# Performance work log

Hardware: AMD Instinct MI355X
Metric: run time of the kernel (lower is better)

## Reference

```python
import jax, jax.numpy as jnp
import numpy as np
import math

F = 64        # num_features (multiplicity of each irrep)
N = 16000     # nodes
E = 256000    # edges (avg_num_neighbors = 16)
S = 4         # num_species
DE = 32       # scalar edge feature dim (radial basis)
W = 128       # interaction_mlp_width
AVG_NEIGH = 16.0
SQ2 = math.sqrt(2.0)
SQ3 = math.sqrt(3.0)


def setup_inputs() -> dict:
    key = jax.random.key(0)
    ks = jax.random.split(key, 32)
    def nrm(k, shape, scale=1.0):
        return jax.random.normal(k, shape, dtype=jnp.float32) * scale
    inp = {}
    # forward args
    inp["vectors"] = nrm(ks[0], (E, 1, 3))
    inp["lengths"] = jax.random.uniform(ks[1], (E, 1), dtype=jnp.float32)
    inp["node_s"] = nrm(ks[2], (N, F))            # 64x0e part of node_feats
    inp["node_v"] = nrm(ks[3], (N, F, 3))         # 64x1o part of node_feats
    inp["scalar_edge_feats"] = nrm(ks[4], (E, DE))
    inp["node_specie"] = jax.random.randint(ks[5], (N,), 0, S)
    inp["senders"] = jax.random.randint(ks[6], (E,), 0, N)
    inp["receivers"] = jax.random.randint(ks[7], (E,), 0, N)
    # parameters (e3nn Linear = per-irrep channel mixing, fan-in normalized; bias only on 0e)
    inp["W_up_s"] = nrm(ks[8], (F, F), F ** -0.5); inp["b_up_s"] = jnp.zeros((F,), jnp.float32)
    inp["W_up_v"] = nrm(ks[9], (F, F), F ** -0.5)
    din = 2 * F + DE + 1
    inp["mlp_W1"] = nrm(ks[10], (din, W), din ** -0.5); inp["mlp_b1"] = jnp.zeros((W,), jnp.float32)
    inp["mlp_W2"] = nrm(ks[11], (W, W), W ** -0.5); inp["mlp_b2"] = jnp.zeros((W,), jnp.float32)
    inp["mlp_W3"] = nrm(ks[12], (W, 3 * F), W ** -0.5); inp["mlp_b3"] = jnp.zeros((3 * F,), jnp.float32)
    inp["W_dn_s"] = nrm(ks[13], (F, F), F ** -0.5); inp["b_dn_s"] = jnp.zeros((F,), jnp.float32)
    inp["W_dn_v"] = nrm(ks[14], (2 * F, F), (2 * F) ** -0.5)
    # symmetric contraction weights (per species, per channel); correlation=2
    inp["w_sc_s"] = nrm(ks[15], (S, 3, F), 3 ** -0.5)   # paths to 0e: x0, x0^2, (x1.x1)/sqrt3
    inp["w_sc_v"] = nrm(ks[16], (S, 2, F), 2 ** -0.5)   # paths to 1o: x1, x0*x1
    inp["W_pb_s"] = nrm(ks[17], (F, F), F ** -0.5); inp["b_pb_s"] = jnp.zeros((F,), jnp.float32)
    inp["W_pb_v"] = nrm(ks[18], (F, F), F ** -0.5)
    inp["W_r1_s"] = nrm(ks[19], (F, 2 * F), F ** -0.5); inp["b_r1_s"] = jnp.zeros((2 * F,), jnp.float32)
    inp["W_r1_v"] = nrm(ks[20], (F, F), F ** -0.5)
    inp["W_r2_s"] = nrm(ks[21], (F, 1), F ** -0.5); inp["b_r2"] = jnp.zeros((1,), jnp.float32)
    inp["W_r2_v"] = nrm(ks[22], (F, 1), F ** -0.5)
    return inp


def reference(vectors, lengths, node_s, node_v, scalar_edge_feats, node_specie,
              senders, receivers,
              W_up_s, b_up_s, W_up_v,
              mlp_W1, mlp_b1, mlp_W2, mlp_b2, mlp_W3, mlp_b3,
              W_dn_s, b_dn_s, W_dn_v,
              w_sc_s, w_sc_v, W_pb_s, b_pb_s, W_pb_v,
              W_r1_s, b_r1_s, W_r1_v, W_r2_s, b_r2, W_r2_v):
    n = node_s.shape[0]
    # --- spherical harmonics, sh_irreps='1o', component normalization, normalize=False ---
    edge_v = SQ3 * vectors[:, 0, :]                              # [E,3]

    # --- InteractionBlock: linear_up ---
    h_s = node_s @ W_up_s + b_up_s                               # [N,F]
    h_v = jnp.einsum('nfi,fg->ngi', node_v, W_up_v)              # [N,F,3]

    # --- MessagePassingConvolution ---
    m_s = h_s[senders]                                           # [E,F] 0e
    m_v = h_v[senders]                                           # [E,F,3] 1o
    # tensor product with edge 1o, filtered to 0e+1o (unitary CG):
    tp_s = jnp.einsum('efi,ei->ef', m_v, edge_v) / SQ3           # 1o x 1o -> 0e  [E,F]
    tp_v1 = m_s[:, :, None] * edge_v[:, None, :]                 # 0e x 1o -> 1o  [E,F,3]
    tp_v2 = jnp.cross(m_v, edge_v[:, None, :]) / SQ2             # 1o x 1o -> 1o  [E,F,3]
    # scalar MLP mix (one scalar weight per output irrep = 3F)
    mlp_in = jnp.concatenate([m_s, h_s[receivers], scalar_edge_feats, lengths], axis=1)
    h = jax.nn.silu(mlp_in @ mlp_W1 + mlp_b1)
    h = jax.nn.silu(h @ mlp_W2 + mlp_b2)
    mix = h @ mlp_W3 + mlp_b3                                    # [E,3F]
    mix_s, mix_v1, mix_v2 = mix[:, :F], mix[:, F:2 * F], mix[:, 2 * F:]
    tp_s = tp_s * mix_s
    tp_v = jnp.concatenate([tp_v1 * mix_v1[:, :, None], tp_v2 * mix_v2[:, :, None]], axis=1)  # [E,2F,3]
    # scatter-add to receivers, normalize by avg_num_neighbors
    agg_s = jax.ops.segment_sum(tp_s, receivers, num_segments=n) / AVG_NEIGH   # [N,F]
    agg_v = jax.ops.segment_sum(tp_v, receivers, num_segments=n) / AVG_NEIGH   # [N,2F,3]
    # linear_down
    f_s = agg_s @ W_dn_s + b_dn_s                                # [N,F]
    f_v = jnp.einsum('nfi,fg->ngi', agg_v, W_dn_v)               # [N,F,3]

    # --- EquivariantProductBasisBlock: symmetric contraction (correlation=2), per-species ---
    ws = w_sc_s[node_specie]                                     # [N,3,F]
    wv = w_sc_v[node_specie]                                     # [N,2,F]
    vv = jnp.sum(f_v * f_v, axis=-1) / SQ3                       # 1o (x) 1o -> 0e, symmetric
    sc_s = ws[:, 0] * f_s + ws[:, 1] * (f_s * f_s) + ws[:, 2] * vv           # [N,F]
    sc_v = wv[:, 0][:, :, None] * f_v + wv[:, 1][:, :, None] * (f_s[:, :, None] * f_v)  # [N,F,3]
    p_s = sc_s @ W_pb_s + b_pb_s                                 # node_feats 0e out
    p_v = jnp.einsum('nfi,fg->ngi', sc_v, W_pb_v)                # node_feats 1o out

    # --- NonLinearReadoutBlock: linear to (2F x 0e + F x 1o), gate, linear to 1x0e+1x1o ---
    r_s = p_s @ W_r1_s + b_r1_s                                  # [N,2F]
    r_v = jnp.einsum('nfi,fg->ngi', p_v, W_r1_v)                 # [N,F,3]
    act = jax.nn.silu(r_s[:, :F])
    gates = jax.nn.silu(r_s[:, F:])
    g_v = gates[:, :, None] * r_v                                # gated vectors
    out_s = act @ W_r2_s + b_r2                                  # [N,1]  0e output
    out_v = jnp.einsum('nfi,fo->noi', g_v, W_r2_v)               # [N,1,3] 1o output
    return out_s, out_v, p_s, p_v
```

## Files before the change

### kernel.cpp

```cpp
#include <hip/hip_runtime.h>

typedef short bf16x8 __attribute__((ext_vector_type(8)));
typedef float f32x4  __attribute__((ext_vector_type(4)));
typedef unsigned short ushort_t;

__device__ __forceinline__ float silu(float x) {
    float t = __expf(-x);
    return x * __builtin_amdgcn_rcpf(1.f + t);
}

__device__ __forceinline__ ushort_t f2bs(float x) {
    union { float f; unsigned int u; } v; v.f = x;
    unsigned int r = v.u + 0x7FFF + ((v.u >> 16) & 1);
    return (ushort_t)(r >> 16);
}
__device__ __forceinline__ ushort_t f2bs_t(float x) {
    union { float f; unsigned int u; } v; v.f = x;
    return (ushort_t)(v.u >> 16);
}
__device__ __forceinline__ float bs2f(ushort_t x) {
    union { unsigned int u; float f; } v; v.u = ((unsigned int)x) << 16; return v.f;
}

#define BAR_LGKM() do { \
    asm volatile("s_waitcnt lgkmcnt(0)" ::: "memory"); \
    __builtin_amdgcn_s_barrier(); \
} while (0)

constexpr int N_   = 16000;
constexpr int E_   = 256000;
constexpr int Fd   = 64;

constexpr float SQ3f    = 1.7320508075688772f;
constexpr float INV_SQ3 = 0.5773502691896258f;
constexpr float INV_SQ2 = 0.7071067811865476f;
constexpr float INV_AVG = 0.0625f;

constexpr int OFF_OS = 0;
constexpr int OFF_OV = N_;
constexpr int OFF_PS = OFF_OV + 3 * N_;
constexpr int OFF_PV = OFF_PS + N_ * Fd;

constexpr int W1P_SZ = 6 * 8 * 512;
constexpr int W2P_SZ = 4 * 8 * 512;
constexpr int W3P_SZ = 4 * 12 * 512;

constexpr int AGG_W = 448;

constexpr int H2_OFF = 8704;

__global__ __launch_bounds__(256) void pack_kernel(
    const float* __restrict__ W1, const float* __restrict__ W2,
    const float* __restrict__ W3,
    ushort_t* __restrict__ W1p, ushort_t* __restrict__ W2p,
    ushort_t* __restrict__ W3p)
{
    int idx = blockIdx.x * 256 + threadIdx.x;
    if (idx < W1P_SZ) {
        int j = idx & 7, lane = (idx >> 3) & 63, tile = idx >> 9;
        int c = tile >> 3, t = tile & 7;
        int k = c * 32 + (lane >> 4) * 8 + j;
        int n = t * 16 + (lane & 15);
        W1p[idx] = f2bs(k < 161 ? W1[k * 128 + n] : 0.f);
    } else if (idx < W1P_SZ + W2P_SZ) {
        int q = idx - W1P_SZ;
        int j = q & 7, lane = (q >> 3) & 63, tile = q >> 9;
        int c = tile >> 3, t = tile & 7;
        int k = c * 32 + (lane >> 4) * 8 + j;
        int n = t * 16 + (lane & 15);
        W2p[q] = f2bs(W2[k * 128 + n]);
    } else {
        int q = idx - W1P_SZ - W2P_SZ;
        int j = q & 7, lane = (q >> 3) & 63, tile = q >> 9;
        int c = tile / 12, t = tile % 12;
        int k = c * 32 + (lane >> 4) * 8 + j;
        int n = t * 16 + (lane & 15);
        W3p[q] = f2bs(W3[k * 192 + n]);
    }
}

__global__ __launch_bounds__(64, 4) void up_kernel(
    const float* __restrict__ node_s, const float* __restrict__ node_v,
    const float* __restrict__ W_up_s, const float* __restrict__ b_up_s,
    const float* __restrict__ W_up_v,
    const int* __restrict__ receivers, int* __restrict__ cnt,
    ushort_t* __restrict__ hs_bf, float* __restrict__ h_v)
{
    __shared__ float ns[4][64];
    __shared__ float nv[4][64][3];
    const int n0 = blockIdx.x * 4;
    const int g  = threadIdx.x;

    {
        int e = blockIdx.x * 64 + g;
        atomicAdd(&cnt[receivers[e]], 1);
    }

    #pragma unroll
    for (int j = 0; j < 4; j++) ns[j][g] = node_s[(n0 + j) * 64 + g];
    for (int idx = g; idx < 4 * 192; idx += 64) {
        int j = idx / 192, r = idx - j * 192;
        nv[j][r / 3][r % 3] = node_v[(size_t)n0 * 192 + idx];
    }
    __syncthreads();

    float as[4], a0[4], a1[4], a2[4];
    float bb = b_up_s[g];
    #pragma unroll
    for (int j = 0; j < 4; j++) { as[j] = bb; a0[j] = a1[j] = a2[j] = 0.f; }
    #pragma unroll 4
    for (int f = 0; f < 64; f++) {
        float wss = W_up_s[f * 64 + g];
        float wv  = W_up_v[f * 64 + g];
        #pragma unroll
        for (int j = 0; j < 4; j++) {
            as[j] += ns[j][f] * wss;
            a0[j] += nv[j][f][0] * wv;
            a1[j] += nv[j][f][1] * wv;
            a2[j] += nv[j][f][2] * wv;
        }
    }
    #pragma unroll
    for (int j = 0; j < 4; j++) {
        hs_bf[(n0 + j) * 64 + g] = f2bs(as[j]);
        h_v[(n0 + j) * 192 + 0 * 64 + g] = a0[j];
        h_v[(n0 + j) * 192 + 1 * 64 + g] = a1[j];
        h_v[(n0 + j) * 192 + 2 * 64 + g] = a2[j];
    }
}

__global__ __launch_bounds__(1024) void scan_kernel(
    const int* __restrict__ cnt, int* __restrict__ base, int* __restrict__ cursor)
{
    __shared__ int part[1024];
    const int t = threadIdx.x;
    int v[16];
    int s = 0;
    if (t < 1000) {
        const int4* c4 = (const int4*)(cnt + t * 16);
        #pragma unroll
        for (int q = 0; q < 4; q++) {
            int4 w = c4[q];
            v[q * 4 + 0] = w.x; v[q * 4 + 1] = w.y;
            v[q * 4 + 2] = w.z; v[q * 4 + 3] = w.w;
            s += w.x + w.y + w.z + w.w;
        }
    }
    part[t] = s;
    __syncthreads();
    for (int off = 1; off < 1024; off <<= 1) {
        int u = (t >= off) ? part[t - off] : 0;
        __syncthreads();
        part[t] += u;
        __syncthreads();
    }
    if (t < 1000) {
        int run = part[t] - s;
        int b[16];
        #pragma unroll
        for (int i = 0; i < 16; i++) { b[i] = run; run += v[i]; }
        int4* bb = (int4*)(base + t * 16);
        int4* cc = (int4*)(cursor + t * 16);
        #pragma unroll
        for (int q = 0; q < 4; q++) {
            int4 w = { b[q * 4], b[q * 4 + 1], b[q * 4 + 2], b[q * 4 + 3] };
            bb[q] = w;
            cc[q] = w;
        }
    }
}

__global__ __launch_bounds__(256) void perm_kernel(
    const int* __restrict__ receivers, int* __restrict__ cursor,
    int* __restrict__ eid)
{
    int e = blockIdx.x * 256 + threadIdx.x;
    int r = receivers[e];
    int p = atomicAdd(&cursor[r], 1);
    eid[p] = e;
}

__global__ __launch_bounds__(256, 4) void edge_mlp_kernel(
    const float* __restrict__ lengths, const float* __restrict__ sef,
    const int* __restrict__ senders, const int* __restrict__ receivers,
    const float* __restrict__ vectors, const int* __restrict__ eid,
    const float* __restrict__ b1f, const float* __restrict__ b2f,
    const float* __restrict__ b3f,
    const ushort_t* __restrict__ hs_bf, const float* __restrict__ h_v,
    const ushort_t* __restrict__ W1p, const ushort_t* __restrict__ W2p,
    const ushort_t* __restrict__ W3p,
    float* __restrict__ agg)
{
    __shared__ ushort_t U[17408];
    __shared__ int snd_s[64];
    __shared__ int rcv_s[64];
    __shared__ float ev_s[64][3];

    const int tid  = threadIdx.x;
    const int wave = tid >> 6, lane = tid & 63;
    const int quad = lane >> 4, l4 = lane & 15;
    const int e0   = blockIdx.x * 64;

    if (tid < 64) {
        int e = eid[e0 + tid];
        snd_s[tid] = senders[e];
        rcv_s[tid] = receivers[e];
        ev_s[tid][0] = SQ3f * vectors[e * 3 + 0];
        ev_s[tid][1] = SQ3f * vectors[e * 3 + 1];
        ev_s[tid][2] = SQ3f * vectors[e * 3 + 2];
    }

    {
        const int e  = tid & 63;
        const int ge = eid[e0 + e];
        const int snd = senders[ge];
        const int rcv = receivers[ge];
        for (int c = tid >> 6; c < 24; c += 4) {
            bf16x8 v;
            if (c < 8) {
                v = *(const bf16x8*)(hs_bf + snd * 64 + c * 8);
            } else if (c < 16) {
                v = *(const bf16x8*)(hs_bf + rcv * 64 + (c - 8) * 8);
            } else if (c < 20) {
                const float4 s0 = *(const float4*)(sef + (size_t)ge * 32 + (c - 16) * 8);
                const float4 s1 = *(const float4*)(sef + (size_t)ge * 32 + (c - 16) * 8 + 4);
                v[0] = (short)f2bs(s0.x); v[1] = (short)f2bs(s0.y);
                v[2] = (short)f2bs(s0.z); v[3] = (short)f2bs(s0.w);
                v[4] = (short)f2bs(s1.x); v[5] = (short)f2bs(s1.y);
                v[6] = (short)f2bs(s1.z); v[7] = (short)f2bs(s1.w);
            } else if (c == 20) {
                v = (bf16x8){0,0,0,0,0,0,0,0};
                v[0] = (short)f2bs(lengths[ge]);
            } else {
                v = (bf16x8){0,0,0,0,0,0,0,0};
            }
            *(bf16x8*)(&U[e * 200 + c * 8]) = v;
        }
    }
    BAR_LGKM();

    const bf16x8* B1 = (const bf16x8*)W1p;
    const bf16x8* B2 = (const bf16x8*)W2p;
    const bf16x8* B3 = (const bf16x8*)W3p;

    {
        f32x4 acc[2][4];
        #pragma unroll
        for (int ti = 0; ti < 2; ti++)
            #pragma unroll
            for (int m = 0; m < 4; m++) acc[ti][m] = (f32x4){0,0,0,0};
        #pragma unroll
        for (int c = 0; c < 6; c++) {
            bf16x8 b0 = B1[(c * 8 + wave * 2 + 0) * 64 + lane];
            bf16x8 b1 = B1[(c * 8 + wave * 2 + 1) * 64 + lane];
            #pragma unroll
            for (int m = 0; m < 4; m++) {
                bf16x8 a = *(const bf16x8*)(&U[(m * 16 + l4) * 200 + c * 32 + quad * 8]);
                acc[0][m] = __builtin_amdgcn_mfma_f32_16x16x32_bf16(a, b0, acc[0][m], 0, 0, 0);
                acc[1][m] = __builtin_amdgcn_mfma_f32_16x16x32_bf16(a, b1, acc[1][m], 0, 0, 0);
            }
        }
        BAR_LGKM();
        #pragma unroll
        for (int ti = 0; ti < 2; ti++) {
            int t = wave * 2 + ti;
            float bb = b1f[t * 16 + l4];
            #pragma unroll
            for (int m = 0; m < 4; m++)
                #pragma unroll
                for (int r = 0; r < 4; r++)
                    U[(m * 16 + quad * 4 + r) * 136 + t * 16 + l4] =
                        f2bs_t(silu(acc[ti][m][r] + bb));
        }
    }
    BAR_LGKM();

    {
        f32x4 acc[2][4];
        #pragma unroll
        for (int ti = 0; ti < 2; ti++)
            #pragma unroll
            for (int m = 0; m < 4; m++) acc[ti][m] = (f32x4){0,0,0,0};
        #pragma unroll
        for (int c = 0; c < 4; c++) {
            bf16x8 b0 = B2[(c * 8 + wave * 2 + 0) * 64 + lane];
            bf16x8 b1 = B2[(c * 8 + wave * 2 + 1) * 64 + lane];
            #pragma unroll
            for (int m = 0; m < 4; m++) {
                bf16x8 a = *(const bf16x8*)(&U[(m * 16 + l4) * 136 + c * 32 + quad * 8]);
                acc[0][m] = __builtin_amdgcn_mfma_f32_16x16x32_bf16(a, b0, acc[0][m], 0, 0, 0);
                acc[1][m] = __builtin_amdgcn_mfma_f32_16x16x32_bf16(a, b1, acc[1][m], 0, 0, 0);
            }
        }
        #pragma unroll
        for (int ti = 0; ti < 2; ti++) {
            int t = wave * 2 + ti;
            float bb = b2f[t * 16 + l4];
            #pragma unroll
            for (int m = 0; m < 4; m++)
                #pragma unroll
                for (int r = 0; r < 4; r++)
                    U[H2_OFF + (m * 16 + quad * 4 + r) * 136 + t * 16 + l4] =
                        f2bs_t(silu(acc[ti][m][r] + bb));
        }
    }
    BAR_LGKM();

    {
        f32x4 acc[3][4];
        #pragma unroll
        for (int ti = 0; ti < 3; ti++)
            #pragma unroll
            for (int m = 0; m < 4; m++) acc[ti][m] = (f32x4){0,0,0,0};
        #pragma unroll
        for (int c = 0; c < 4; c++) {
            bf16x8 b0 = B3[(c * 12 + wave * 3 + 0) * 64 + lane];
            bf16x8 b1 = B3[(c * 12 + wave * 3 + 1) * 64 + lane];
            bf16x8 b2 = B3[(c * 12 + wave * 3 + 2) * 64 + lane];
            #pragma unroll
            for (int m = 0; m < 4; m++) {
                bf16x8 a = *(const bf16x8*)(&U[H2_OFF + (m * 16 + l4) * 136 + c * 32 + quad * 8]);
                acc[0][m] = __builtin_amdgcn_mfma_f32_16x16x32_bf16(a, b0, acc[0][m], 0, 0, 0);
                acc[1][m] = __builtin_amdgcn_mfma_f32_16x16x32_bf16(a, b1, acc[1][m], 0, 0, 0);
                acc[2][m] = __builtin_amdgcn_mfma_f32_16x16x32_bf16(a, b2, acc[2][m], 0, 0, 0);
            }
        }
        BAR_LGKM();
        #pragma unroll
        for (int ti = 0; ti < 3; ti++) {
            int t = wave * 3 + ti;
            float bb = b3f[t * 16 + l4];
            #pragma unroll
            for (int m = 0; m < 4; m++)
                #pragma unroll
                for (int r = 0; r < 4; r++)
                    U[(m * 16 + quad * 4 + r) * 200 + t * 16 + l4] =
                        f2bs(acc[ti][m][r] + bb);
        }
    }
    BAR_LGKM();

    {
        const int g  = lane;
        const int p0 = wave * 16;
        float acc0 = 0.f, acc1 = 0.f, acc2 = 0.f, acc3 = 0.f;
        float acc4 = 0.f, acc5 = 0.f, acc6 = 0.f;
        int cur = rcv_s[p0];

        for (int jj = 0; jj < 16; jj += 8) {
            float M0[8], M1[8], M2[8], MS[8];
            #pragma unroll
            for (int j = 0; j < 8; j++) {
                const int se = snd_s[p0 + jj + j];
                M0[j] = h_v[(size_t)se * 192 + 0 * 64 + g];
                M1[j] = h_v[(size_t)se * 192 + 1 * 64 + g];
                M2[j] = h_v[(size_t)se * 192 + 2 * 64 + g];
                MS[j] = bs2f(hs_bf[se * 64 + g]);
            }
            #pragma unroll
            for (int j = 0; j < 8; j++) {
                const int el = p0 + jj + j;
                const int r  = rcv_s[el];
                if (r != cur) {
                    float* a = agg + (size_t)cur * AGG_W + g;
                    atomicAdd(a +   0, acc0); atomicAdd(a +  64, acc1);
                    atomicAdd(a + 128, acc2); atomicAdd(a + 192, acc3);
                    atomicAdd(a + 256, acc4); atomicAdd(a + 320, acc5);
                    atomicAdd(a + 384, acc6);
                    acc0 = acc1 = acc2 = acc3 = acc4 = acc5 = acc6 = 0.f;
                    cur = r;
                }
                const float ev0 = ev_s[el][0], ev1 = ev_s[el][1], ev2 = ev_s[el][2];
                const float mixs  = bs2f(U[el * 200 +   0 + g]);
                const float mixv1 = bs2f(U[el * 200 +  64 + g]);
                const float mixv2 = bs2f(U[el * 200 + 128 + g]);
                const float k = MS[j] * mixv1;
                acc0 += (M0[j] * ev0 + M1[j] * ev1 + M2[j] * ev2) * mixs;
                acc1 += k * ev0;
                acc2 += k * ev1;
                acc3 += k * ev2;
                acc4 += (M1[j] * ev2 - M2[j] * ev1) * mixv2;
                acc5 += (M2[j] * ev0 - M0[j] * ev2) * mixv2;
                acc6 += (M0[j] * ev1 - M1[j] * ev0) * mixv2;
            }
        }
        float* a = agg + (size_t)cur * AGG_W + g;
        atomicAdd(a +   0, acc0); atomicAdd(a +  64, acc1);
        atomicAdd(a + 128, acc2); atomicAdd(a + 192, acc3);
        atomicAdd(a + 256, acc4); atomicAdd(a + 320, acc5);
        atomicAdd(a + 384, acc6);
    }
}

__global__ __launch_bounds__(256, 2) void node_fused_kernel(
    const float* __restrict__ agg,
    const int* __restrict__ specie,
    const float* __restrict__ W_dn_s, const float* __restrict__ b_dn_s,
    const float* __restrict__ W_dn_v,
    const float* __restrict__ w_sc_s, const float* __restrict__ w_sc_v,
    const float* __restrict__ W_pb_s, const float* __restrict__ b_pb_s,
    const float* __restrict__ W_pb_v,
    const float* __restrict__ W_r1_s, const float* __restrict__ b_r1_s,
    const float* __restrict__ W_r1_v,
    const float* __restrict__ W_r2_s, const float* __restrict__ b_r2,
    const float* __restrict__ W_r2_v,
    float* __restrict__ out)
{
    __shared__ float as_l[4][64];
    __shared__ float av_l[4][128][3];
    __shared__ float scs[4][64];
    __shared__ float scv[4][64][3];
    __shared__ float ps_[4][64];
    __shared__ float pv_[4][64][3];

    const int tid = threadIdx.x;
    const int w   = tid >> 6;
    const int g   = tid & 63;
    const int n   = blockIdx.x * 4 + w;

    const float* ag = agg + (size_t)n * AGG_W;
    as_l[w][g]        = ag[g]       * (INV_SQ3 * INV_AVG);
    av_l[w][g][0]     = ag[ 64 + g] * INV_AVG;
    av_l[w][g][1]     = ag[128 + g] * INV_AVG;
    av_l[w][g][2]     = ag[192 + g] * INV_AVG;
    av_l[w][64 + g][0] = ag[256 + g] * (INV_SQ2 * INV_AVG);
    av_l[w][64 + g][1] = ag[320 + g] * (INV_SQ2 * INV_AVG);
    av_l[w][64 + g][2] = ag[384 + g] * (INV_SQ2 * INV_AVG);

    float f_s = b_dn_s[g];
    #pragma unroll 8
    for (int f = 0; f < 64; f++) f_s += as_l[w][f] * W_dn_s[f * 64 + g];
    float fv0 = 0.f, fv1 = 0.f, fv2 = 0.f;
    #pragma unroll 8
    for (int f = 0; f < 128; f++) {
        float wt = W_dn_v[f * 64 + g];
        fv0 += av_l[w][f][0] * wt;
        fv1 += av_l[w][f][1] * wt;
        fv2 += av_l[w][f][2] * wt;
    }

    float vv = (fv0 * fv0 + fv1 * fv1 + fv2 * fv2) * INV_SQ3;
    int sp = specie[n];
    float ws0 = w_sc_s[sp * 192 + 0 * 64 + g];
    float ws1 = w_sc_s[sp * 192 + 1 * 64 + g];
    float ws2 = w_sc_s[sp * 192 + 2 * 64 + g];
    float wv0 = w_sc_v[sp * 128 + 0 * 64 + g];
    float wv1 = w_sc_v[sp * 128 + 1 * 64 + g];
    float sc_s = ws0 * f_s + ws1 * f_s * f_s + ws2 * vv;
    float kv = wv0 + wv1 * f_s;
    scs[w][g] = sc_s;
    scv[w][g][0] = kv * fv0;
    scv[w][g][1] = kv * fv1;
    scv[w][g][2] = kv * fv2;

    float p_s = b_pb_s[g];
    float pv0 = 0.f, pv1 = 0.f, pv2 = 0.f;
    #pragma unroll 8
    for (int f = 0; f < 64; f++) {
        float wps = W_pb_s[f * 64 + g];
        p_s += scs[w][f] * wps;
        float wpv = W_pb_v[f * 64 + g];
        pv0 += scv[w][f][0] * wpv;
        pv1 += scv[w][f][1] * wpv;
        pv2 += scv[w][f][2] * wpv;
    }
    ps_[w][g] = p_s;
    pv_[w][g][0] = pv0; pv_[w][g][1] = pv1; pv_[w][g][2] = pv2;

    out[OFF_PS + n * 64 + g] = p_s;
    out[OFF_PV + (size_t)n * 192 + g * 3 + 0] = pv0;
    out[OFF_PV + (size_t)n * 192 + g * 3 + 1] = pv1;
    out[OFF_PV + (size_t)n * 192 + g * 3 + 2] = pv2;

    float r0 = b_r1_s[g];
    float r1 = b_r1_s[g + 64];
    float rv0 = 0.f, rv1 = 0.f, rv2 = 0.f;
    #pragma unroll 8
    for (int f = 0; f < 64; f++) {
        float p = ps_[w][f];
        r0 += p * W_r1_s[f * 128 + g];
        r1 += p * W_r1_s[f * 128 + g + 64];
        float wrv = W_r1_v[f * 64 + g];
        rv0 += pv_[w][f][0] * wrv;
        rv1 += pv_[w][f][1] * wrv;
        rv2 += pv_[w][f][2] * wrv;
    }
    float act  = silu(r0);
    float gate = silu(r1);
    float o_s = act * W_r2_s[g];
    float wr2v = W_r2_v[g];
    float ov0 = gate * rv0 * wr2v;
    float ov1 = gate * rv1 * wr2v;
    float ov2 = gate * rv2 * wr2v;

    #pragma unroll
    for (int off = 32; off > 0; off >>= 1) {
        o_s += __shfl_down(o_s, off);
        ov0 += __shfl_down(ov0, off);
        ov1 += __shfl_down(ov1, off);
        ov2 += __shfl_down(ov2, off);
    }
    if (g == 0) {
        out[OFF_OS + n] = o_s + b_r2[0];
        out[OFF_OV + n * 3 + 0] = ov0;
        out[OFF_OV + n * 3 + 1] = ov1;
        out[OFF_OV + n * 3 + 2] = ov2;
    }
}

extern "C" void kernel_launch(void* const* d_in, const int* in_sizes, int n_in,
                              void* d_out, int out_size, void* d_ws, size_t ws_size,
                              hipStream_t stream)
{
    const float* vectors  = (const float*)d_in[0];
    const float* lengths  = (const float*)d_in[1];
    const float* node_s   = (const float*)d_in[2];
    const float* node_v   = (const float*)d_in[3];
    const float* sef      = (const float*)d_in[4];
    const int*  specie    = (const int*)d_in[5];
    const int*  senders   = (const int*)d_in[6];
    const int*  receivers = (const int*)d_in[7];
    const float* W_up_s   = (const float*)d_in[8];
    const float* b_up_s   = (const float*)d_in[9];
    const float* W_up_v   = (const float*)d_in[10];
    const float* mlp_W1   = (const float*)d_in[11];
    const float* mlp_b1   = (const float*)d_in[12];
    const float* mlp_W2   = (const float*)d_in[13];
    const float* mlp_b2   = (const float*)d_in[14];
    const float* mlp_W3   = (const float*)d_in[15];
    const float* mlp_b3   = (const float*)d_in[16];
    const float* W_dn_s   = (const float*)d_in[17];
    const float* b_dn_s   = (const float*)d_in[18];
    const float* W_dn_v   = (const float*)d_in[19];
    const float* w_sc_s   = (const float*)d_in[20];
    const float* w_sc_v   = (const float*)d_in[21];
    const float* W_pb_s   = (const float*)d_in[22];
    const float* b_pb_s   = (const float*)d_in[23];
    const float* W_pb_v   = (const float*)d_in[24];
    const float* W_r1_s   = (const float*)d_in[25];
    const float* b_r1_s   = (const float*)d_in[26];
    const float* W_r1_v   = (const float*)d_in[27];
    const float* W_r2_s   = (const float*)d_in[28];
    const float* b_r2     = (const float*)d_in[29];
    const float* W_r2_v   = (const float*)d_in[30];

    float* h_v   = (float*)d_ws;
    float* agg   = h_v + (size_t)N_ * 192;
    ushort_t* hs_bf = (ushort_t*)(agg + (size_t)N_ * AGG_W);
    ushort_t* W1p   = hs_bf + (size_t)N_ * 64;
    ushort_t* W2p   = W1p + W1P_SZ;
    ushort_t* W3p   = W2p + W2P_SZ;
    int* eid        = (int*)((((size_t)(W3p + W3P_SZ)) + 15) & ~(size_t)15);
    int* cnt        = eid + E_;
    int* base       = cnt + N_;
    int* cursor     = base + N_;

    float* out = (float*)d_out;

    hipMemsetAsync(cnt, 0, N_ * sizeof(int), stream);
    hipMemsetAsync(agg, 0, (size_t)N_ * AGG_W * sizeof(float), stream);

    up_kernel<<<N_ / 4, 64, 0, stream>>>(node_s, node_v, W_up_s, b_up_s, W_up_v,
                                         receivers, cnt, hs_bf, h_v);
    pack_kernel<<<256, 256, 0, stream>>>(mlp_W1, mlp_W2, mlp_W3, W1p, W2p, W3p);
    scan_kernel<<<1, 1024, 0, stream>>>(cnt, base, cursor);
    perm_kernel<<<E_ / 256, 256, 0, stream>>>(receivers, cursor, eid);

    edge_mlp_kernel<<<E_ / 64, 256, 0, stream>>>(
        lengths, sef, senders, receivers, vectors, eid,
        mlp_b1, mlp_b2, mlp_b3,
        hs_bf, h_v, W1p, W2p, W3p, agg);

    node_fused_kernel<<<N_ / 4, 256, 0, stream>>>(
        agg, specie,
        W_dn_s, b_dn_s, W_dn_v, w_sc_s, w_sc_v,
        W_pb_s, b_pb_s, W_pb_v, W_r1_s, b_r1_s, W_r1_v,
        W_r2_s, b_r2, W_r2_v, out);
}
```

Baseline: 363.8 us.

## Process four nodes per wave in node kernel to reuse weight loads

The node kernel now has each wavefront handle four nodes instead of one, so every weight element loaded from global memory is reused across four nodes' accumulators. Intermediate activations move into float4-packed shared arrays, which allows vectorized LDS reads, and the shared buffers are reused between stages. The launch grid shrinks by four and launch bounds ask for higher occupancy. The trade-off is more registers per thread, and the node kernel is likely a small part of total time next to the edge MLP kernel.

```diff
diff --git a/kernel.cpp b/kernel.cpp
--- a/kernel.cpp
+++ b/kernel.cpp
@@ -392,7 +392,7 @@
     }
 }
 
-__global__ __launch_bounds__(256, 2) void node_fused_kernel(
+__global__ __launch_bounds__(256, 4) void node_fused_kernel(
     const float* __restrict__ agg,
     const int* __restrict__ specie,
     const float* __restrict__ W_dn_s, const float* __restrict__ b_dn_s,
@@ -406,105 +406,140 @@
     const float* __restrict__ W_r2_v,
     float* __restrict__ out)
 {
-    __shared__ float as_l[4][64];
-    __shared__ float av_l[4][128][3];
-    __shared__ float scs[4][64];
-    __shared__ float scv[4][64][3];
-    __shared__ float ps_[4][64];
-    __shared__ float pv_[4][64][3];
+    __shared__ float4 LD[16][64];
+    __shared__ float4 LE[16][64];
 
     const int tid = threadIdx.x;
     const int w   = tid >> 6;
     const int g   = tid & 63;
-    const int n   = blockIdx.x * 4 + w;
-
-    const float* ag = agg + (size_t)n * AGG_W;
-    as_l[w][g]        = ag[g]       * (INV_SQ3 * INV_AVG);
-    av_l[w][g][0]     = ag[ 64 + g] * INV_AVG;
-    av_l[w][g][1]     = ag[128 + g] * INV_AVG;
-    av_l[w][g][2]     = ag[192 + g] * INV_AVG;
-    av_l[w][64 + g][0] = ag[256 + g] * (INV_SQ2 * INV_AVG);
-    av_l[w][64 + g][1] = ag[320 + g] * (INV_SQ2 * INV_AVG);
-    av_l[w][64 + g][2] = ag[384 + g] * (INV_SQ2 * INV_AVG);
-
-    float f_s = b_dn_s[g];
-    #pragma unroll 8
-    for (int f = 0; f < 64; f++) f_s += as_l[w][f] * W_dn_s[f * 64 + g];
-    float fv0 = 0.f, fv1 = 0.f, fv2 = 0.f;
-    #pragma unroll 8
-    for (int f = 0; f < 128; f++) {
-        float wt = W_dn_v[f * 64 + g];
-        fv0 += av_l[w][f][0] * wt;
-        fv1 += av_l[w][f][1] * wt;
-        fv2 += av_l[w][f][2] * wt;
-    }
-
-    float vv = (fv0 * fv0 + fv1 * fv1 + fv2 * fv2) * INV_SQ3;
-    int sp = specie[n];
-    float ws0 = w_sc_s[sp * 192 + 0 * 64 + g];
-    float ws1 = w_sc_s[sp * 192 + 1 * 64 + g];
-    float ws2 = w_sc_s[sp * 192 + 2 * 64 + g];
-    float wv0 = w_sc_v[sp * 128 + 0 * 64 + g];
-    float wv1 = w_sc_v[sp * 128 + 1 * 64 + g];
-    float sc_s = ws0 * f_s + ws1 * f_s * f_s + ws2 * vv;
-    float kv = wv0 + wv1 * f_s;
-    scs[w][g] = sc_s;
-    scv[w][g][0] = kv * fv0;
-    scv[w][g][1] = kv * fv1;
-    scv[w][g][2] = kv * fv2;
-
-    float p_s = b_pb_s[g];
-    float pv0 = 0.f, pv1 = 0.f, pv2 = 0.f;
-    #pragma unroll 8
+    const int nb  = blockIdx.x * 16 + w * 4;
+    const int r0i = w * 4;
+
+    #pragma unroll
+    for (int j = 0; j < 4; j++) {
+        const float* ag = agg + (size_t)(nb + j) * AGG_W;
+        float a0 = ag[g], a1 = ag[64 + g], a2 = ag[128 + g], a3 = ag[192 + g];
+        float b1 = ag[256 + g], b2 = ag[320 + g], b3 = ag[384 + g];
+        LD[r0i + j][g] = make_float4(a0 * (INV_SQ3 * INV_AVG),
+                                     a1 * INV_AVG, a2 * INV_AVG, a3 * INV_AVG);
+        LE[r0i + j][g] = make_float4(0.f,
+                                     b1 * (INV_SQ2 * INV_AVG),
+                                     b2 * (INV_SQ2 * INV_AVG),
+                                     b3 * (INV_SQ2 * INV_AVG));
+    }
+
+    float fs[4], fv0[4], fv1[4], fv2[4];
+    {
+        float bds = b_dn_s[g];
+        #pragma unroll
+        for (int j = 0; j < 4; j++) { fs[j] = bds; fv0[j] = fv1[j] = fv2[j] = 0.f; }
+    }
+    #pragma unroll 4
+    for (int f = 0; f < 64; f++) {
+        float ws  = W_dn_s[f * 64 + g];
+        float wva = W_dn_v[f * 64 + g];
+        float wvb = W_dn_v[(64 + f) * 64 + g];
+        #pragma unroll
+        for (int j = 0; j < 4; j++) {
+            float4 a = LD[r0i + j][f];
+            float4 b = LE[r0i + j][f];
+            fs[j]  += a.x * ws;
+            fv0[j] += a.y * wva + b.y * wvb;
+            fv1[j] += a.z * wva + b.z * wvb;
+            fv2[j] += a.w * wva + b.w * wvb;
+        }
+    }
+
+    #pragma unroll
+    for (int j = 0; j < 4; j++) {
+        int sp = specie[nb + j];
+        float vv = (fv0[j] * fv0[j] + fv1[j] * fv1[j] + fv2[j] * fv2[j]) * INV_SQ3;
+        float ws0 = w_sc_s[sp * 192 +   0 + g];
+        float ws1 = w_sc_s[sp * 192 +  64 + g];
+        float ws2 = w_sc_s[sp * 192 + 128 + g];
+        float wv0 = w_sc_v[sp * 128 +   0 + g];
+        float wv1 = w_sc_v[sp * 128 +  64 + g];
+        float sc_s = ws0 * fs[j] + ws1 * fs[j] * fs[j] + ws2 * vv;
+        float kv = wv0 + wv1 * fs[j];
+        LD[r0i + j][g] = make_float4(sc_s, kv * fv0[j], kv * fv1[j], kv * fv2[j]);
+    }
+
+    float ps[4], pv0[4], pv1[4], pv2[4];
+    {
+        float bpb = b_pb_s[g];
+        #pragma unroll
+        for (int j = 0; j < 4; j++) { ps[j] = bpb; pv0[j] = pv1[j] = pv2[j] = 0.f; }
+    }
+    #pragma unroll 4
     for (int f = 0; f < 64; f++) {
         float wps = W_pb_s[f * 64 + g];
-        p_s += scs[w][f] * wps;
         float wpv = W_pb_v[f * 64 + g];
-        pv0 += scv[w][f][0] * wpv;
-        pv1 += scv[w][f][1] * wpv;
-        pv2 += scv[w][f][2] * wpv;
-    }
-    ps_[w][g] = p_s;
-    pv_[w][g][0] = pv0; pv_[w][g][1] = pv1; pv_[w][g][2] = pv2;
-
-    out[OFF_PS + n * 64 + g] = p_s;
-    out[OFF_PV + (size_t)n * 192 + g * 3 + 0] = pv0;
-    out[OFF_PV + (size_t)n * 192 + g * 3 + 1] = pv1;
-    out[OFF_PV + (size_t)n * 192 + g * 3 + 2] = pv2;
-
-    float r0 = b_r1_s[g];
-    float r1 = b_r1_s[g + 64];
-    float rv0 = 0.f, rv1 = 0.f, rv2 = 0.f;
-    #pragma unroll 8
+        #pragma unroll
+        for (int j = 0; j < 4; j++) {
+            float4 s = LD[r0i + j][f];
+            ps[j]  += s.x * wps;
+            pv0[j] += s.y * wpv;
+            pv1[j] += s.z * wpv;
+            pv2[j] += s.w * wpv;
+        }
+    }
+    #pragma unroll
+    for (int j = 0; j < 4; j++) {
+        LE[r0i + j][g] = make_float4(ps[j], pv0[j], pv1[j], pv2[j]);
+        out[OFF_PS + (nb + j) * 64 + g] = ps[j];
+        out[OFF_PV + (size_t)(nb + j) * 192 + g * 3 + 0] = pv0[j];
+        out[OFF_PV + (size_t)(nb + j) * 192 + g * 3 + 1] = pv1[j];
+        out[OFF_PV + (size_t)(nb + j) * 192 + g * 3 + 2] = pv2[j];
+    }
+
+    float ra[4], rb[4], rv0[4], rv1[4], rv2[4];
+    {
+        float br0 = b_r1_s[g];
+        float br1 = b_r1_s[g + 64];
+        #pragma unroll
+        for (int j = 0; j < 4; j++) { ra[j] = br0; rb[j] = br1; rv0[j] = rv1[j] = rv2[j] = 0.f; }
+    }
+    #pragma unroll 4
     for (int f = 0; f < 64; f++) {
-        float p = ps_[w][f];
-        r0 += p * W_r1_s[f * 128 + g];
-        r1 += p * W_r1_s[f * 128 + g + 64];
+        float w0  = W_r1_s[f * 128 + g];
+        float w1  = W_r1_s[f * 128 + g + 64];
         float wrv = W_r1_v[f * 64 + g];
-        rv0 += pv_[w][f][0] * wrv;
-        rv1 += pv_[w][f][1] * wrv;
-        rv2 += pv_[w][f][2] * wrv;
-    }
-    float act  = silu(r0);
-    float gate = silu(r1);
-    float o_s = act * W_r2_s[g];
-    float wr2v = W_r2_v[g];
-    float ov0 = gate * rv0 * wr2v;
-    float ov1 = gate * rv1 * wr2v;
-    float ov2 = gate * rv2 * wr2v;
-
-    #pragma unroll
-    for (int off = 32; off > 0; off >>= 1) {
-        o_s += __shfl_down(o_s, off);
-        ov0 += __shfl_down(ov0, off);
-        ov1 += __shfl_down(ov1, off);
-        ov2 += __shfl_down(ov2, off);
-    }
-    if (g == 0) {
-        out[OFF_OS + n] = o_s + b_r2[0];
-        out[OFF_OV + n * 3 + 0] = ov0;
-        out[OFF_OV + n * 3 + 1] = ov1;
-        out[OFF_OV + n * 3 + 2] = ov2;
+        #pragma unroll
+        for (int j = 0; j < 4; j++) {
+            float4 p = LE[r0i + j][f];
+            ra[j]  += p.x * w0;
+            rb[j]  += p.x * w1;
+            rv0[j] += p.y * wrv;
+            rv1[j] += p.z * wrv;
+            rv2[j] += p.w * wrv;
+        }
+    }
+    {
+        float wr2s = W_r2_s[g];
+        float wr2v = W_r2_v[g];
+        float br2  = b_r2[0];
+        #pragma unroll
+        for (int j = 0; j < 4; j++) {
+            float act  = silu(ra[j]);
+            float gate = silu(rb[j]);
+            float o_s = act * wr2s;
+            float ov0 = gate * rv0[j] * wr2v;
+            float ov1 = gate * rv1[j] * wr2v;
+            float ov2 = gate * rv2[j] * wr2v;
+            #pragma unroll
+            for (int off = 32; off > 0; off >>= 1) {
+                o_s += __shfl_down(o_s, off);
+                ov0 += __shfl_down(ov0, off);
+                ov1 += __shfl_down(ov1, off);
+                ov2 += __shfl_down(ov2, off);
+            }
+            if (g == 0) {
+                out[OFF_OS + (nb + j)] = o_s + br2;
+                out[OFF_OV + (nb + j) * 3 + 0] = ov0;
+                out[OFF_OV + (nb + j) * 3 + 1] = ov1;
+                out[OFF_OV + (nb + j) * 3 + 2] = ov2;
+            }
+        }
     }
 }
 
@@ -571,7 +606,7 @@
         mlp_b1, mlp_b2, mlp_b3,
         hs_bf, h_v, W1p, W2p, W3p, agg);
 
-    node_fused_kernel<<<N_ / 4, 256, 0, stream>>>(
+    node_fused_kernel<<<N_ / 16, 256, 0, stream>>>(
         agg, specie,
         W_dn_s, b_dn_s, W_dn_v, w_sc_s, w_sc_v,
         W_pb_s, b_pb_s, W_pb_v, W_r1_s, b_r1_s, W_r1_v,
```

Result: faster. 354.0 us (-2.7%).
